# Kernel optimization log

Hardware: AMD Instinct MI355X
Metric: run time of the kernel (lower is better)

Reference implementation:

```python
import jax, jax.numpy as jnp
import numpy as np

EPS = 1e-5

def layer_norm(x, gamma, beta):
    mu = jnp.mean(x, axis=-1, keepdims=True)
    var = jnp.var(x, axis=-1, keepdims=True)
    return (x - mu) * jax.lax.rsqrt(var + EPS) * gamma + beta

def setup_inputs() -> dict:
    key = jax.random.key(0)
    ks = jax.random.split(key, 8)
    T, B, E, H, K = 2048, 2, 1024, 16, 64
    x = jax.random.normal(ks[0], (T, B, E), dtype=jnp.float32)
    # causal mask: 0 where allowed (s<=t), -1e9 where masked
    attn_mask = jnp.where(jnp.tril(jnp.ones((T, T), dtype=bool)), 0.0, -1e9).astype(jnp.float32)
    def xavier(k, shape, gain):
        fan_out, fan_in = shape
        std = gain * np.sqrt(2.0 / (fan_in + fan_out))
        return (jax.random.normal(k, shape, dtype=jnp.float32) * std)
    Wq = xavier(ks[1], (H * K, E), 1.0)
    Wk = xavier(ks[2], (K, E), 1.0)
    Wv = xavier(ks[3], (E, E), 1.0)
    return {
        'x': x, 'attn_mask': attn_mask,
        'Wq': Wq, 'bq': jnp.zeros((H * K,), jnp.float32),
        'Wk': Wk, 'bk': jnp.zeros((K,), jnp.float32),
        'Wv': Wv, 'bv': jnp.zeros((E,), jnp.float32),
        'k_gamma': jnp.ones((K,), jnp.float32), 'k_beta': jnp.zeros((K,), jnp.float32),
        'v_gamma': jnp.ones((E,), jnp.float32), 'v_beta': jnp.zeros((E,), jnp.float32),
    }

def reference(x, attn_mask, Wq, bq, Wk, bk, Wv, bv, k_gamma, k_beta, v_gamma, v_beta):
    T, B, E = x.shape
    K = Wk.shape[0]
    H = Wq.shape[0] // K
    q = (x @ Wq.T + bq).reshape(T, B, H, K)          # [T,B,H,K]
    k = layer_norm(x @ Wk.T + bk, k_gamma, k_beta)   # [T,B,K]
    v = layer_norm(x @ Wv.T + bv, v_gamma, v_beta)   # [T,B,E]
    # outer-product state per step, then causal cumulative sum.
    # einsum('ts,sbkd->tbkd', scaling*causal_mask, s) == cumsum over s<=t,
    # scaled per query position t by (t+1)^-0.5 (mask is causal lower-tri).
    outer = jnp.einsum('tbk,tbd->tbkd', k, v)        # [T,B,K,E]
    s = jnp.cumsum(outer, axis=0)
    scaling = jax.lax.rsqrt(jnp.arange(1, T + 1, dtype=x.dtype))
    s = s * scaling[:, None, None, None]
    qn = jnp.mean(jax.nn.softmax(q, axis=-1), axis=2)  # [T,B,K] (dropout_p=0, eval)
    attn = jnp.einsum('tbk,tbkd->tbd', qn, s)          # [T,B,E]
    return attn
```

## Files before the change

### kernel.cpp

```cpp
#include <hip/hip_runtime.h>
#include <math.h>

#define T_DIM 2048
#define B_DIM 2
#define E_DIM 1024
#define K_DIM 64
#define H_DIM 16
#define R_DIM (T_DIM * B_DIM)
#define WROWS 2176
#define NCH 16

typedef __bf16 bf16x8 __attribute__((ext_vector_type(8)));
typedef __bf16 bf16x4 __attribute__((ext_vector_type(4)));
typedef float f32x4 __attribute__((ext_vector_type(4)));

#define GLD16(gptr, lptr)                                                      \
    __builtin_amdgcn_global_load_lds(                                          \
        (const __attribute__((address_space(1))) void*)(gptr),                 \
        (__attribute__((address_space(3))) void*)(lptr), 16, 0, 0)

__global__ __launch_bounds__(256) void cvt_all(const float* __restrict__ X,
                                               const float* __restrict__ Wq,
                                               const float* __restrict__ Wv,
                                               const float* __restrict__ Wk,
                                               __bf16* __restrict__ XB,
                                               __bf16* __restrict__ WB) {
    const size_t nq = (size_t)1024 * 1024;
    const size_t nk = (size_t)64 * 1024;
    bf16x8 o;
    if (blockIdx.x < 2048) {
        size_t g = ((size_t)blockIdx.x * 256 + threadIdx.x) * 8;
        float4 a = *(const float4*)&X[g];
        float4 b = *(const float4*)&X[g + 4];
        o[0] = (__bf16)a.x; o[1] = (__bf16)a.y; o[2] = (__bf16)a.z; o[3] = (__bf16)a.w;
        o[4] = (__bf16)b.x; o[5] = (__bf16)b.y; o[6] = (__bf16)b.z; o[7] = (__bf16)b.w;
        *(bf16x8*)&XB[g] = o;
    } else {
        size_t g = ((size_t)(blockIdx.x - 2048) * 256 + threadIdx.x) * 8;
        if (g < 2 * nq + nk) {
            const float* src;
            size_t off;
            if (g < nq)          { src = Wq; off = g; }
            else if (g < 2 * nq) { src = Wv; off = g - nq; }
            else                 { src = Wk; off = g - 2 * nq; }
            float4 a = *(const float4*)&src[off];
            float4 b = *(const float4*)&src[off + 4];
            o[0] = (__bf16)a.x; o[1] = (__bf16)a.y; o[2] = (__bf16)a.z; o[3] = (__bf16)a.w;
            o[4] = (__bf16)b.x; o[5] = (__bf16)b.y; o[6] = (__bf16)b.z; o[7] = (__bf16)b.w;
        } else {
#pragma unroll
            for (int i = 0; i < 8; ++i) o[i] = (__bf16)0.f;
        }
        *(bf16x8*)&WB[g] = o;
    }
}

__global__ __launch_bounds__(256) void gemm_mfma(const __bf16* __restrict__ XB,
                                                 const __bf16* __restrict__ WB,
                                                 const float* __restrict__ bq,
                                                 const float* __restrict__ bv,
                                                 const float* __restrict__ bk,
                                                 __bf16* __restrict__ Qb,
                                                 __bf16* __restrict__ Vb,
                                                 float* __restrict__ Kr) {
    __shared__ __bf16 Als[128 * 32];
    __shared__ __bf16 Bls[128 * 32];
    const int tid = threadIdx.x;
    const int lane = tid & 63;
    const int w = tid >> 6;
    const int wm = (w & 1) * 64;
    const int wn = (w >> 1) * 64;
    const int rBase = blockIdx.x * 128;
    const int cBase = blockIdx.y * 128;

    const int c0 = tid, c1 = tid + 256;
    const __bf16* gA0 = XB + (size_t)(rBase + (c0 >> 2)) * E_DIM + (c0 & 3) * 8;
    const __bf16* gA1 = XB + (size_t)(rBase + (c1 >> 2)) * E_DIM + (c1 & 3) * 8;
    const __bf16* gB0 = WB + (size_t)(cBase + (c0 >> 2)) * E_DIM + (c0 & 3) * 8;
    const __bf16* gB1 = WB + (size_t)(cBase + (c1 >> 2)) * E_DIM + (c1 & 3) * 8;
    __bf16* lA0 = Als + c0 * 8;
    __bf16* lA1 = Als + c1 * 8;
    __bf16* lB0 = Bls + c0 * 8;
    __bf16* lB1 = Bls + c1 * 8;

    const int fr = lane & 15;
    const int fk = (lane >> 4) * 8;
    const __bf16* aF = Als + (wm + fr) * 32 + fk;
    const __bf16* bF = Bls + (wn + fr) * 32 + fk;

    f32x4 acc[4][4] = {};

    for (int kk = 0; kk < E_DIM; kk += 32) {
        __syncthreads();
        GLD16(gA0 + kk, lA0);
        GLD16(gA1 + kk, lA1);
        GLD16(gB0 + kk, lB0);
        GLD16(gB1 + kk, lB1);
        __syncthreads();

        bf16x8 af[4], bfr[4];
#pragma unroll
        for (int mt = 0; mt < 4; ++mt) af[mt] = *(const bf16x8*)(aF + mt * 16 * 32);
#pragma unroll
        for (int nt = 0; nt < 4; ++nt) bfr[nt] = *(const bf16x8*)(bF + nt * 16 * 32);
#pragma unroll
        for (int mt = 0; mt < 4; ++mt)
#pragma unroll
            for (int nt = 0; nt < 4; ++nt)
                acc[mt][nt] = __builtin_amdgcn_mfma_f32_16x16x32_bf16(
                    af[mt], bfr[nt], acc[mt][nt], 0, 0, 0);
    }

    const int row0 = rBase + wm + (lane >> 4) * 4;
    if (cBase < 2048) {
        const float* bias;
        __bf16* Cout;
        int colBase;
        if (cBase < 1024) { bias = bq; Cout = Qb; colBase = cBase; }
        else              { bias = bv; Cout = Vb; colBase = cBase - 1024; }
        const int col0 = colBase + wn + (lane & 15);
#pragma unroll
        for (int mt = 0; mt < 4; ++mt)
#pragma unroll
            for (int nt = 0; nt < 4; ++nt) {
                int cc = col0 + nt * 16;
                float bb = bias[cc];
#pragma unroll
                for (int r = 0; r < 4; ++r)
                    Cout[(size_t)(row0 + mt * 16 + r) * E_DIM + cc] =
                        (__bf16)(acc[mt][nt][r] + bb);
            }
    } else {
        const int col0 = wn + (lane & 15);
#pragma unroll
        for (int mt = 0; mt < 4; ++mt)
#pragma unroll
            for (int nt = 0; nt < 4; ++nt) {
                int cc = col0 + nt * 16;
                if (cc < 64) {
                    float bb = bk[cc];
#pragma unroll
                    for (int r = 0; r < 4; ++r)
                        Kr[(size_t)(row0 + mt * 16 + r) * K_DIM + cc] =
                            acc[mt][nt][r] + bb;
                }
            }
    }
}

__global__ __launch_bounds__(256) void rowops(const __bf16* __restrict__ Qb,
                                              const float* __restrict__ Kraw,
                                              const __bf16* __restrict__ Vb,
                                              const float* __restrict__ kg,
                                              const float* __restrict__ kb,
                                              __bf16* __restrict__ QNB,
                                              __bf16* __restrict__ KNB,
                                              float2* __restrict__ ST) {
    const int r = blockIdx.x;
    const int tid = threadIdx.x;
    const int lane = tid & 63, wv = tid >> 6;
    const int t = r >> 1, b = r & 1;
    __shared__ float redq[4][64];
    __shared__ float redv[2][4];

    float acc = 0.f;
#pragma unroll
    for (int h4 = 0; h4 < 4; ++h4) {
        int h = wv * 4 + h4;
        float v = (float)Qb[(size_t)r * 1024 + h * 64 + lane];
        float m = v;
#pragma unroll
        for (int off = 32; off; off >>= 1) m = fmaxf(m, __shfl_xor(m, off));
        float e = expf(v - m);
        float ssum = e;
#pragma unroll
        for (int off = 32; off; off >>= 1) ssum += __shfl_xor(ssum, off);
        acc += e / ssum;
    }
    redq[wv][lane] = acc;

    {
        bf16x4 v4 = *(const bf16x4*)&Vb[(size_t)r * 1024 + tid * 4];
        float a = (float)v4[0], c = (float)v4[1], d = (float)v4[2], e = (float)v4[3];
        float s = a + c + d + e;
        float s2 = a * a + c * c + d * d + e * e;
#pragma unroll
        for (int off = 32; off; off >>= 1) {
            s += __shfl_xor(s, off);
            s2 += __shfl_xor(s2, off);
        }
        if (lane == 0) { redv[0][wv] = s; redv[1][wv] = s2; }
    }
    __syncthreads();

    if (tid < 64) {
        float s = redq[0][tid] + redq[1][tid] + redq[2][tid] + redq[3][tid];
        QNB[((size_t)b * T_DIM + t) * K_DIM + tid] = (__bf16)(s * (1.f / 16.f));
    } else if (tid < 128) {
        float v = Kraw[(size_t)r * K_DIM + lane];
        float s = v, s2 = v * v;
#pragma unroll
        for (int off = 32; off; off >>= 1) {
            s += __shfl_xor(s, off);
            s2 += __shfl_xor(s2, off);
        }
        float mean = s * (1.f / 64.f);
        float var = s2 * (1.f / 64.f) - mean * mean;
        float inv = rsqrtf(var + 1e-5f);
        KNB[((size_t)b * T_DIM + t) * K_DIM + lane] =
            (__bf16)((v - mean) * inv * kg[lane] + kb[lane]);
    } else if (tid == 128) {
        float s = redv[0][0] + redv[0][1] + redv[0][2] + redv[0][3];
        float s2 = redv[1][0] + redv[1][1] + redv[1][2] + redv[1][3];
        float mean = s * (1.f / 1024.f);
        float var = s2 * (1.f / 1024.f) - mean * mean;
        ST[r] = make_float2(mean, rsqrtf(var + 1e-5f));
    }
}

__global__ __launch_bounds__(256) void prep_lnT(const __bf16* __restrict__ VB,
                                                const float2* __restrict__ ST,
                                                const float* __restrict__ gamma,
                                                const float* __restrict__ beta,
                                                __bf16* __restrict__ VT) {
    __shared__ float tile[64][65];
    const int bid = blockIdx.x;
    const int tid = threadIdx.x;
    const int tb = bid & 31, eb = (bid >> 5) & 15, b = bid >> 9;
#pragma unroll
    for (int j = 0; j < 2; ++j) {
        int idx = tid + j * 256;
        int tl = idx >> 3, e8 = idx & 7;
        int r = (tb * 64 + tl) * B_DIM + b;
        float2 st = ST[r];
        bf16x8 v = *(const bf16x8*)&VB[(size_t)r * E_DIM + eb * 64 + e8 * 8];
#pragma unroll
        for (int i = 0; i < 8; ++i)
            tile[tl][e8 * 8 + i] = ((float)v[i] - st.x) * st.y;
    }
    __syncthreads();
#pragma unroll
    for (int j = 0; j < 4; ++j) {
        int idx = tid + j * 256;
        int e = idx >> 4, t4 = idx & 15;
        float g = gamma[eb * 64 + e], bb = beta[eb * 64 + e];
        bf16x4 o;
#pragma unroll
        for (int i = 0; i < 4; ++i) o[i] = (__bf16)(tile[t4 * 4 + i][e] * g + bb);
        *(bf16x4*)&VT[((size_t)b * E_DIM + eb * 64 + e) * T_DIM + tb * 64 + t4 * 4] = o;
    }
}

__global__ __launch_bounds__(256) void stateU(const __bf16* __restrict__ VT,
                                              const __bf16* __restrict__ KNB,
                                              float* __restrict__ U) {
    __shared__ __bf16 Als[64 * 32];
    __shared__ __bf16 knT[64 * 136];
    const int c = blockIdx.x, b = blockIdx.y, eq = blockIdx.z;
    const int tid = threadIdx.x;
    const int lane = tid & 63;
    const int w = tid >> 6;
    const int fr = lane & 15;
    const int quad = lane >> 4;

    {
        int s = tid >> 1, kh = (tid & 1) * 32;
        const __bf16* src = KNB + ((size_t)b * T_DIM + c * 128 + s) * K_DIM + kh;
#pragma unroll
        for (int i8 = 0; i8 < 4; ++i8) {
            bf16x8 v = *(const bf16x8*)&src[i8 * 8];
#pragma unroll
            for (int i = 0; i < 8; ++i) knT[(kh + i8 * 8 + i) * 136 + s] = v[i];
        }
    }

    const int e0 = eq * 64;
    const __bf16* vtb = VT + ((size_t)b * E_DIM + e0) * T_DIM + c * 128;
    f32x4 acc[4] = {};

    for (int kit = 0; kit < 4; ++kit) {
        __syncthreads();
        {
            int row = tid >> 2, part = tid & 3;
            GLD16(vtb + (size_t)row * T_DIM + kit * 32 + part * 8, &Als[tid * 8]);
        }
        __syncthreads();
        bf16x8 af = *(const bf16x8*)&Als[(w * 16 + fr) * 32 + quad * 8];
        bf16x8 bfr[4];
#pragma unroll
        for (int nt = 0; nt < 4; ++nt)
            bfr[nt] = *(const bf16x8*)&knT[(nt * 16 + fr) * 136 + kit * 32 + quad * 8];
#pragma unroll
        for (int nt = 0; nt < 4; ++nt)
            acc[nt] = __builtin_amdgcn_mfma_f32_16x16x32_bf16(
                af, bfr[nt], acc[nt], 0, 0, 0);
    }

    float* ub = U + ((size_t)(c * 2 + b) * 1024 + e0) * K_DIM;
#pragma unroll
    for (int nt = 0; nt < 4; ++nt) {
        int k = nt * 16 + fr;
#pragma unroll
        for (int r = 0; r < 4; ++r)
            ub[(size_t)(w * 16 + quad * 4 + r) * K_DIM + k] = acc[nt][r];
    }
}

__global__ __launch_bounds__(256) void scanS(const float* __restrict__ U,
                                             __bf16* __restrict__ Shi,
                                             __bf16* __restrict__ Slo) {
    const size_t idx = (size_t)blockIdx.x * 256 + threadIdx.x;
    float run = 0.f;
#pragma unroll
    for (int c = 0; c < NCH; ++c) {
        __bf16 h = (__bf16)run;
        Shi[(size_t)c * 131072 + idx] = h;
        Slo[(size_t)c * 131072 + idx] = (__bf16)(run - (float)h);
        run += U[(size_t)c * 131072 + idx];
    }
}

__global__ __launch_bounds__(256) void outPV(const __bf16* __restrict__ QNB,
                                             const __bf16* __restrict__ KNB,
                                             const __bf16* __restrict__ VT,
                                             const __bf16* __restrict__ Shi,
                                             const __bf16* __restrict__ Slo,
                                             float* __restrict__ OUT) {
    __shared__ __align__(16) __bf16 qns[128 * 72];
    __shared__ __align__(16) __bf16 Pl[128 * 136];
    __shared__ __align__(16) __bf16 Vls[128 * 32];
    const int c = blockIdx.x, b = blockIdx.y, eo = blockIdx.z;
    const int tid = threadIdx.x;
    const int lane = tid & 63;
    const int w = tid >> 6;
    const int fr = lane & 15;
    const int quad = lane >> 4;

#pragma unroll
    for (int j = 0; j < 4; ++j) {
        int idx = tid + j * 256;
        int row = idx >> 3, k8 = idx & 7;
        *(bf16x8*)&qns[row * 72 + k8 * 8] =
            *(const bf16x8*)&QNB[((size_t)b * T_DIM + c * 128 + row) * K_DIM + k8 * 8];
    }
    __syncthreads();

    const __bf16* knc = KNB + ((size_t)b * T_DIM + c * 128) * K_DIM;
    {
        f32x4 pacc[8][2] = {};
#pragma unroll
        for (int kit = 0; kit < 2; ++kit) {
            bf16x8 bq[2];
#pragma unroll
            for (int nt = 0; nt < 2; ++nt) {
                int q = w * 32 + nt * 16 + fr;
                bq[nt] = *(const bf16x8*)&qns[q * 72 + kit * 32 + quad * 8];
            }
#pragma unroll
            for (int mt = 0; mt < 8; ++mt) {
                bf16x8 af = *(const bf16x8*)&knc[(size_t)(mt * 16 + fr) * K_DIM +
                                                 kit * 32 + quad * 8];
#pragma unroll
                for (int nt = 0; nt < 2; ++nt)
                    pacc[mt][nt] = __builtin_amdgcn_mfma_f32_16x16x32_bf16(
                        af, bq[nt], pacc[mt][nt], 0, 0, 0);
            }
        }
#pragma unroll
        for (int mt = 0; mt < 8; ++mt)
#pragma unroll
            for (int nt = 0; nt < 2; ++nt) {
                int q = w * 32 + nt * 16 + fr;
                int s0 = mt * 16 + quad * 4;
                bf16x4 o;
#pragma unroll
                for (int r = 0; r < 4; ++r) {
                    float val = pacc[mt][nt][r];
                    if (s0 + r > q) val = 0.f;
                    o[r] = (__bf16)val;
                }
                *(bf16x4*)&Pl[q * 136 + s0] = o;
            }
    }
    __syncthreads();

    const int we = (w & 1) * 64, wt = (w >> 1) * 64;
    const int e0 = eo * 128;
    f32x4 acc[4][4] = {};

    if (c > 0) {
        const __bf16* sh = Shi + (size_t)c * 131072 + ((size_t)b * 1024 + e0 + we) * K_DIM;
        const __bf16* sl = Slo + (size_t)c * 131072 + ((size_t)b * 1024 + e0 + we) * K_DIM;
#pragma unroll
        for (int kit = 0; kit < 2; ++kit) {
            bf16x8 bq[4];
#pragma unroll
            for (int nt = 0; nt < 4; ++nt) {
                int t = wt + nt * 16 + fr;
                bq[nt] = *(const bf16x8*)&qns[t * 72 + kit * 32 + quad * 8];
            }
#pragma unroll
            for (int mt = 0; mt < 4; ++mt) {
                size_t ro = (size_t)(mt * 16 + fr) * K_DIM + kit * 32 + quad * 8;
                bf16x8 ah = *(const bf16x8*)&sh[ro];
                bf16x8 al = *(const bf16x8*)&sl[ro];
#pragma unroll
                for (int nt = 0; nt < 4; ++nt) {
                    acc[mt][nt] = __builtin_amdgcn_mfma_f32_16x16x32_bf16(
                        ah, bq[nt], acc[mt][nt], 0, 0, 0);
                    acc[mt][nt] = __builtin_amdgcn_mfma_f32_16x16x32_bf16(
                        al, bq[nt], acc[mt][nt], 0, 0, 0);
                }
            }
        }
    }

    const __bf16* vtb = VT + ((size_t)b * E_DIM + e0) * T_DIM + c * 128;
    for (int kit = 0; kit < 4; ++kit) {
        __syncthreads();
#pragma unroll
        for (int j = 0; j < 2; ++j) {
            int g = tid + j * 256;
            int row = g >> 2, part = g & 3;
            GLD16(vtb + (size_t)row * T_DIM + kit * 32 + part * 8, &Vls[g * 8]);
        }
        __syncthreads();
        bf16x8 av[4], bp[4];
#pragma unroll
        for (int mt = 0; mt < 4; ++mt)
            av[mt] = *(const bf16x8*)&Vls[(we + mt * 16 + fr) * 32 + quad * 8];
#pragma unroll
        for (int nt = 0; nt < 4; ++nt)
            bp[nt] = *(const bf16x8*)&Pl[(wt + nt * 16 + fr) * 136 + kit * 32 + quad * 8];
#pragma unroll
        for (int mt = 0; mt < 4; ++mt)
#pragma unroll
            for (int nt = 0; nt < 4; ++nt)
                acc[mt][nt] = __builtin_amdgcn_mfma_f32_16x16x32_bf16(
                    av[mt], bp[nt], acc[mt][nt], 0, 0, 0);
    }
    __syncthreads();

    float* tb = (float*)qns + w * 1280;
#pragma unroll
    for (int mt = 0; mt < 4; ++mt) {
#pragma unroll
        for (int nt = 0; nt < 4; ++nt)
            *(f32x4*)&tb[(nt * 16 + fr) * 20 + quad * 4] = acc[mt][nt];
#pragma unroll
        for (int j = 0; j < 4; ++j) {
            int fid = lane + j * 64;
            int trow = fid >> 2, e4 = fid & 3;
            float4 val = *(const float4*)&tb[trow * 20 + e4 * 4];
            int t = c * 128 + wt + trow;
            float sca = rsqrtf((float)(t + 1));
            float4 r = {val.x * sca, val.y * sca, val.z * sca, val.w * sca};
            *(float4*)&OUT[((size_t)t * B_DIM + b) * E_DIM + e0 + we + mt * 16 + e4 * 4] = r;
        }
    }
}

extern "C" void kernel_launch(void* const* d_in, const int* in_sizes, int n_in,
                              void* d_out, int out_size, void* d_ws,
                              size_t ws_size, hipStream_t stream) {
    const float* x = (const float*)d_in[0];
    const float* Wq = (const float*)d_in[2];
    const float* bq = (const float*)d_in[3];
    const float* Wk = (const float*)d_in[4];
    const float* bk = (const float*)d_in[5];
    const float* Wv = (const float*)d_in[6];
    const float* bv = (const float*)d_in[7];
    const float* kg = (const float*)d_in[8];
    const float* kb = (const float*)d_in[9];
    const float* vg = (const float*)d_in[10];
    const float* vb = (const float*)d_in[11];
    float* out = (float*)d_out;

    char* base = (char*)d_ws;
    const size_t MB = 1024 * 1024;
    __bf16* qb    = (__bf16*)(base + 0);
    __bf16* vbuf  = (__bf16*)(base + 8 * MB);
    float*  kraw  = (float*)(base + 16 * MB);
    __bf16* xb    = (__bf16*)(base + 17 * MB);
    __bf16* wb    = (__bf16*)(base + 25 * MB);
    __bf16* qnb   = (__bf16*)(base + 30 * MB);
    __bf16* knb   = (__bf16*)(base + 31 * MB);
    float2* stats = (float2*)(base + 32 * MB);
    float*  Ubuf = (float*)(base + 0);
    __bf16* Shi  = (__bf16*)(base + 8 * MB);
    __bf16* Slo  = (__bf16*)(base + 12 * MB);
    __bf16* vbT  = xb;

    cvt_all<<<dim3(2048 + WROWS * 1024 / 2048), 256, 0, stream>>>(x, Wq, Wv, Wk, xb, wb);
    gemm_mfma<<<dim3(32, 17), 256, 0, stream>>>(xb, wb, bq, bv, bk, qb, vbuf, kraw);
    rowops<<<dim3(R_DIM), 256, 0, stream>>>(qb, kraw, vbuf, kg, kb, qnb, knb, stats);
    prep_lnT<<<dim3(1024), 256, 0, stream>>>(vbuf, stats, vg, vb, vbT);
    stateU<<<dim3(NCH, 2, 16), 256, 0, stream>>>(vbT, knb, Ubuf);
    scanS<<<dim3(512), 256, 0, stream>>>(Ubuf, Shi, Slo);
    outPV<<<dim3(NCH, 2, 8), 256, 0, stream>>>(qnb, knb, vbT, Shi, Slo, out);
}
```

Measured before the change: 175.0 us.

## Fuse V layernorm-transpose into state kernel and remap GEMM block order

Merges the prep_lnT kernel into stateU so each block normalizes and transposes its V tile into shared memory and uses it directly for the MFMA state computation. The transposed V is still written to global memory for the later outPV kernel. This removes one kernel launch and the global re-read of the transposed V. The GEMM grid is also flattened and block indices remapped, likely to spread row/column tiles across XCDs for better L2 reuse. The fused kernel uses more shared memory and has lower parallelism: 512 blocks now do what 1024 plus 512 blocks did before.

```diff
diff --git a/kernel.cpp b/kernel.cpp
--- a/kernel.cpp
+++ b/kernel.cpp
@@ -65,13 +65,17 @@
                                                  float* __restrict__ Kr) {
     __shared__ __bf16 Als[128 * 32];
     __shared__ __bf16 Bls[128 * 32];
+    const int bid = blockIdx.x;
+    const int v = (bid & 7) * 68 + (bid >> 3);
+    const int bx = v / 17;
+    const int by = v % 17;
     const int tid = threadIdx.x;
     const int lane = tid & 63;
     const int w = tid >> 6;
     const int wm = (w & 1) * 64;
     const int wn = (w >> 1) * 64;
-    const int rBase = blockIdx.x * 128;
-    const int cBase = blockIdx.y * 128;
+    const int rBase = bx * 128;
+    const int cBase = by * 128;
 
     const int c0 = tid, c1 = tid + 256;
     const __bf16* gA0 = XB + (size_t)(rBase + (c0 >> 2)) * E_DIM + (c0 & 3) * 8;
@@ -218,74 +222,67 @@
     }
 }
 
-__global__ __launch_bounds__(256) void prep_lnT(const __bf16* __restrict__ VB,
-                                                const float2* __restrict__ ST,
-                                                const float* __restrict__ gamma,
-                                                const float* __restrict__ beta,
-                                                __bf16* __restrict__ VT) {
+__global__ __launch_bounds__(256) void lnT_stateU(const __bf16* __restrict__ VB,
+                                                  const float2* __restrict__ ST,
+                                                  const float* __restrict__ gamma,
+                                                  const float* __restrict__ beta,
+                                                  const __bf16* __restrict__ KNB,
+                                                  __bf16* __restrict__ VT,
+                                                  float* __restrict__ U) {
     __shared__ float tile[64][65];
-    const int bid = blockIdx.x;
-    const int tid = threadIdx.x;
-    const int tb = bid & 31, eb = (bid >> 5) & 15, b = bid >> 9;
-#pragma unroll
-    for (int j = 0; j < 2; ++j) {
-        int idx = tid + j * 256;
-        int tl = idx >> 3, e8 = idx & 7;
-        int r = (tb * 64 + tl) * B_DIM + b;
-        float2 st = ST[r];
-        bf16x8 v = *(const bf16x8*)&VB[(size_t)r * E_DIM + eb * 64 + e8 * 8];
-#pragma unroll
-        for (int i = 0; i < 8; ++i)
-            tile[tl][e8 * 8 + i] = ((float)v[i] - st.x) * st.y;
-    }
-    __syncthreads();
-#pragma unroll
-    for (int j = 0; j < 4; ++j) {
-        int idx = tid + j * 256;
-        int e = idx >> 4, t4 = idx & 15;
-        float g = gamma[eb * 64 + e], bb = beta[eb * 64 + e];
-        bf16x4 o;
-#pragma unroll
-        for (int i = 0; i < 4; ++i) o[i] = (__bf16)(tile[t4 * 4 + i][e] * g + bb);
-        *(bf16x4*)&VT[((size_t)b * E_DIM + eb * 64 + e) * T_DIM + tb * 64 + t4 * 4] = o;
-    }
-}
-
-__global__ __launch_bounds__(256) void stateU(const __bf16* __restrict__ VT,
-                                              const __bf16* __restrict__ KNB,
-                                              float* __restrict__ U) {
-    __shared__ __bf16 Als[64 * 32];
     __shared__ __bf16 knT[64 * 136];
+    __shared__ __bf16 VTl[64 * 136];
     const int c = blockIdx.x, b = blockIdx.y, eq = blockIdx.z;
     const int tid = threadIdx.x;
     const int lane = tid & 63;
     const int w = tid >> 6;
     const int fr = lane & 15;
     const int quad = lane >> 4;
+    const int e0 = eq * 64;
 
     {
         int s = tid >> 1, kh = (tid & 1) * 32;
         const __bf16* src = KNB + ((size_t)b * T_DIM + c * 128 + s) * K_DIM + kh;
 #pragma unroll
         for (int i8 = 0; i8 < 4; ++i8) {
-            bf16x8 v = *(const bf16x8*)&src[i8 * 8];
-#pragma unroll
-            for (int i = 0; i < 8; ++i) knT[(kh + i8 * 8 + i) * 136 + s] = v[i];
-        }
-    }
-
-    const int e0 = eq * 64;
-    const __bf16* vtb = VT + ((size_t)b * E_DIM + e0) * T_DIM + c * 128;
+            bf16x8 vv = *(const bf16x8*)&src[i8 * 8];
+#pragma unroll
+            for (int i = 0; i < 8; ++i) knT[(kh + i8 * 8 + i) * 136 + s] = vv[i];
+        }
+    }
+
+#pragma unroll
+    for (int th = 0; th < 2; ++th) {
+#pragma unroll
+        for (int j = 0; j < 2; ++j) {
+            int idx = tid + j * 256;
+            int tl = idx >> 3, e8 = idx & 7;
+            int r = (c * 128 + th * 64 + tl) * B_DIM + b;
+            float2 st = ST[r];
+            bf16x8 vv = *(const bf16x8*)&VB[(size_t)r * E_DIM + e0 + e8 * 8];
+#pragma unroll
+            for (int i = 0; i < 8; ++i)
+                tile[tl][e8 * 8 + i] = ((float)vv[i] - st.x) * st.y;
+        }
+        __syncthreads();
+#pragma unroll
+        for (int j = 0; j < 4; ++j) {
+            int idx = tid + j * 256;
+            int e = idx >> 4, t4 = idx & 15;
+            float g = gamma[e0 + e], bb = beta[e0 + e];
+            bf16x4 o;
+#pragma unroll
+            for (int i = 0; i < 4; ++i) o[i] = (__bf16)(tile[t4 * 4 + i][e] * g + bb);
+            *(bf16x4*)&VT[((size_t)b * E_DIM + e0 + e) * T_DIM + c * 128 + th * 64 + t4 * 4] = o;
+            *(bf16x4*)&VTl[e * 136 + th * 64 + t4 * 4] = o;
+        }
+        __syncthreads();
+    }
+
     f32x4 acc[4] = {};
-
+#pragma unroll
     for (int kit = 0; kit < 4; ++kit) {
-        __syncthreads();
-        {
-            int row = tid >> 2, part = tid & 3;
-            GLD16(vtb + (size_t)row * T_DIM + kit * 32 + part * 8, &Als[tid * 8]);
-        }
-        __syncthreads();
-        bf16x8 af = *(const bf16x8*)&Als[(w * 16 + fr) * 32 + quad * 8];
+        bf16x8 af = *(const bf16x8*)&VTl[(w * 16 + fr) * 136 + kit * 32 + quad * 8];
         bf16x8 bfr[4];
 #pragma unroll
         for (int nt = 0; nt < 4; ++nt)
@@ -492,10 +489,9 @@
     __bf16* vbT  = xb;
 
     cvt_all<<<dim3(2048 + WROWS * 1024 / 2048), 256, 0, stream>>>(x, Wq, Wv, Wk, xb, wb);
-    gemm_mfma<<<dim3(32, 17), 256, 0, stream>>>(xb, wb, bq, bv, bk, qb, vbuf, kraw);
+    gemm_mfma<<<dim3(544), 256, 0, stream>>>(xb, wb, bq, bv, bk, qb, vbuf, kraw);
     rowops<<<dim3(R_DIM), 256, 0, stream>>>(qb, kraw, vbuf, kg, kb, qnb, knb, stats);
-    prep_lnT<<<dim3(1024), 256, 0, stream>>>(vbuf, stats, vg, vb, vbT);
-    stateU<<<dim3(NCH, 2, 16), 256, 0, stream>>>(vbT, knb, Ubuf);
+    lnT_stateU<<<dim3(NCH, 2, 16), 256, 0, stream>>>(vbuf, stats, vg, vb, knb, vbT, Ubuf);
     scanS<<<dim3(512), 256, 0, stream>>>(Ubuf, Shi, Slo);
     outPV<<<dim3(NCH, 2, 8), 256, 0, stream>>>(qnb, knb, vbT, Shi, Slo, out);
 }
```

Measured after the change: 172.7 us (median of 2 runs). No clear change (-1.3%).
